# Kernel optimization log

Hardware: AMD Instinct MI355X
Metric: run time of the kernel (lower is better)

Reference implementation:

```python
import jax, jax.numpy as jnp
import numpy as np

EPS = 1e-6      # zero-token detection eps
LN_EPS = 1e-5   # torch LayerNorm default
H = 8           # num_heads


def setup_inputs() -> dict:
    key = jax.random.key(0)
    ks = jax.random.split(key, 6)
    B, T, D = 4, 2048, 512
    embs = jax.random.normal(ks[0], (B, T, D), jnp.float32)
    labels = jax.random.uniform(ks[1], (B, T), jnp.float32)
    s = 1.0 / np.sqrt(D)
    ln_g = jnp.ones((D,), jnp.float32)
    ln_b = jnp.zeros((D,), jnp.float32)
    in_proj_w = jax.random.uniform(ks[2], (3 * D, D), jnp.float32, -s, s)
    in_proj_b = jnp.zeros((3 * D,), jnp.float32)
    out_w = jax.random.uniform(ks[3], (D, D), jnp.float32, -s, s)
    out_b = jnp.zeros((D,), jnp.float32)
    alpha = jnp.float32(1.0)
    beta = jnp.float32(0.0)
    return {"embs": embs, "labels": labels, "ln_g": ln_g, "ln_b": ln_b,
            "in_proj_w": in_proj_w, "in_proj_b": in_proj_b,
            "out_w": out_w, "out_b": out_b, "alpha": alpha, "beta": beta}


def reference(embs, labels, ln_g, ln_b, in_proj_w, in_proj_b, out_w, out_b, alpha, beta):
    B, T, D = embs.shape
    h, dh = H, D // H
    # pre-LayerNorm
    mu = embs.mean(-1, keepdims=True)
    var = ((embs - mu) ** 2).mean(-1, keepdims=True)
    x = (embs - mu) / jnp.sqrt(var + LN_EPS) * ln_g + ln_b
    # key padding mask from all-zero tokens (computed on normalized x, as in source)
    kpm = jnp.abs(x).sum(-1) <= EPS                      # [B,T] bool
    w = jnp.where(kpm, jnp.float32(0.0), labels)         # zero labels on masked tokens
    # fused qkv projection (nn.MultiheadAttention in_proj)
    qkv = x @ in_proj_w.T + in_proj_b                    # [B,T,3D]
    q, k, v = jnp.split(qkv, 3, axis=-1)
    def sp(a):
        return a.reshape(B, T, h, dh).transpose(0, 2, 1, 3)  # [B,h,T,dh]
    q, k, v = sp(q), sp(k), sp(v)
    scores = jnp.einsum('bhqd,bhkd->bhqk', q, k) / np.sqrt(dh)
    # additive label bias: alpha * labels (broadcast over heads & queries) + beta
    scores = scores + (alpha * w[:, None, None, :] + beta)
    # key padding mask -> -inf (use large negative for stability)
    scores = jnp.where(kpm[:, None, None, :], jnp.float32(-1e30), scores)
    a = jax.nn.softmax(scores, axis=-1)
    o = jnp.einsum('bhqk,bhkd->bhqd', a, v).transpose(0, 2, 1, 3).reshape(B, T, D)
    o = o @ out_w.T + out_b
    o = jnp.nan_to_num(o, nan=0.0, posinf=0.0, neginf=0.0)
    # masked mean pool over T
    m = (~kpm)[..., None].astype(o.dtype)                # [B,T,1]
    pooled = (o * m).sum(1) / jnp.maximum(m.sum(1), 1.0)  # [B,D]
    return pooled
```

## Files before the change

### kernel.cpp

```cpp
#include <hip/hip_runtime.h>
#include <math.h>

#define T 2048
#define D 512
#define NH 8
#define DH 64
#define NB 4
#define NTOK (NB * T)
#define LOG2E 1.44269504f
#define QSCALE (0.125f * LOG2E)

using bf16x8 = __attribute__((ext_vector_type(8))) short;
using f32x4  = __attribute__((ext_vector_type(4))) float;

static __device__ __forceinline__ unsigned short f2bf(float f) {
    union { float f; unsigned u; } v; v.f = f;
    unsigned r = v.u + 0x7fffu + ((v.u >> 16) & 1u);
    return (unsigned short)(r >> 16);
}
#if __has_builtin(__builtin_amdgcn_cvt_pk_bf16_f32)
static __device__ __forceinline__ unsigned pack_bf16_pair(float a, float b) {
    auto r = __builtin_amdgcn_cvt_pk_bf16_f32(a, b);
    union { decltype(r) v; unsigned u; } c; c.v = r;
    return c.u;
}
#else
static __device__ __forceinline__ unsigned pack_bf16_pair(float a, float b) {
    union { float f; unsigned u; } ua, ub; ua.f = a; ub.f = b;
    unsigned ra = ua.u + 0x7fffu + ((ua.u >> 16) & 1u);
    unsigned rb = ub.u + 0x7fffu + ((ub.u >> 16) & 1u);
    return __builtin_amdgcn_perm(rb, ra, 0x07060302);
}
#endif


__global__ __launch_bounds__(256) void prep_kernel(
    const float* __restrict__ embs, const float* __restrict__ labels,
    const float* __restrict__ g, const float* __restrict__ bb,
    const float* __restrict__ alpha_p, const float* __restrict__ beta_p,
    const float* __restrict__ ipw,
    unsigned short* __restrict__ xfrag, float* __restrict__ wexp,
    float* __restrict__ kpmf, unsigned short* __restrict__ wbfrag,
    float* __restrict__ S)
{
    __shared__ __align__(16) unsigned short Sh[16][520];
    int blk = blockIdx.x;
    int tid = threadIdx.x, wave = tid >> 6, lane = tid & 63;
    int quad = lane >> 4, lm = lane & 15;

    if (blk >= 608) {
        float4 z = {0.f, 0.f, 0.f, 0.f};
        ((float4*)S)[tid] = z;
        ((float4*)S)[tid + 256] = z;
        return;
    }

    if (blk < 512) {
        int t16 = blk;
        float4 g0 = *(const float4*)(g + lane * 8), g1 = *(const float4*)(g + lane * 8 + 4);
        float4 c0 = *(const float4*)(bb + lane * 8), c1 = *(const float4*)(bb + lane * 8 + 4);
        float gv[8] = {g0.x, g0.y, g0.z, g0.w, g1.x, g1.y, g1.z, g1.w};
        float cv[8] = {c0.x, c0.y, c0.z, c0.w, c1.x, c1.y, c1.z, c1.w};

        for (int tt = 0; tt < 4; ++tt) {
            int n = t16 * 16 + wave * 4 + tt;
            const float* e = embs + (size_t)n * D + lane * 8;
            float4 a4 = *(const float4*)e, b4 = *(const float4*)(e + 4);
            float v[8] = {a4.x, a4.y, a4.z, a4.w, b4.x, b4.y, b4.z, b4.w};

            float s = 0.f, ss = 0.f;
            #pragma unroll
            for (int j = 0; j < 8; ++j) { s += v[j]; ss += v[j] * v[j]; }
            #pragma unroll
            for (int o = 1; o <= 32; o <<= 1) {
                s += __shfl_xor(s, o, 64);
                ss += __shfl_xor(ss, o, 64);
            }
            float mu = s * (1.0f / D);
            float var = ss * (1.0f / D) - mu * mu;
            float rstd = rsqrtf(var + 1e-5f);

            float x[8], as = 0.f;
            #pragma unroll
            for (int j = 0; j < 8; ++j) {
                x[j] = (v[j] - mu) * rstd * gv[j] + cv[j];
                as += fabsf(x[j]);
            }
            uint4 pk;
            pk.x = pack_bf16_pair(x[0], x[1]);
            pk.y = pack_bf16_pair(x[2], x[3]);
            pk.z = pack_bf16_pair(x[4], x[5]);
            pk.w = pack_bf16_pair(x[6], x[7]);
            *(uint4*)&Sh[wave * 4 + tt][lane * 8] = pk;

            #pragma unroll
            for (int o = 1; o <= 32; o <<= 1) as += __shfl_xor(as, o, 64);
            if (lane == 0) {
                int kpm = (as <= 1e-6f);
                kpmf[n] = kpm ? 1.0f : 0.0f;
                wexp[n] = kpm ? 0.0f : __expf(alpha_p[0] * labels[n] + beta_p[0]);
            }
        }
        __syncthreads();
        #pragma unroll
        for (int i = 0; i < 4; ++i) {
            int kc = wave * 4 + i;
            bf16x8 fr = *(const bf16x8*)&Sh[lm][kc * 32 + quad * 8];
            *(bf16x8*)(xfrag + ((size_t)(t16 * 16 + kc) * 64 + lane) * 8) = fr;
        }
    } else {
        int j16 = blk - 512;
        for (int tt = 0; tt < 4; ++tt) {
            int j = j16 * 16 + wave * 4 + tt;
            const float* wp = ipw + (size_t)j * D + lane * 8;
            float4 a4 = *(const float4*)wp, b4 = *(const float4*)(wp + 4);
            uint4 pk;
            pk.x = pack_bf16_pair(a4.x, a4.y);
            pk.y = pack_bf16_pair(a4.z, a4.w);
            pk.z = pack_bf16_pair(b4.x, b4.y);
            pk.w = pack_bf16_pair(b4.z, b4.w);
            *(uint4*)&Sh[wave * 4 + tt][lane * 8] = pk;
        }
        __syncthreads();
        #pragma unroll
        for (int i = 0; i < 4; ++i) {
            int kc = wave * 4 + i;
            bf16x8 fr = *(const bf16x8*)&Sh[lm][kc * 32 + quad * 8];
            *(bf16x8*)(wbfrag + ((size_t)(j16 * 16 + kc) * 64 + lane) * 8) = fr;
        }
    }
}

union QkvLds {
    struct { unsigned short A[2][8][512]; unsigned short B[2][8][512]; } st;
    unsigned short Ls[4][64][72];
};
__global__ __launch_bounds__(256) void qkv_mfma(
    const unsigned short* __restrict__ xfrag, const unsigned short* __restrict__ wbfrag,
    const float* __restrict__ bias, const float* __restrict__ wexp,
    unsigned short* __restrict__ qfrag, unsigned short* __restrict__ kfrag,
    unsigned short* __restrict__ vfrag)
{
    __shared__ __align__(16) QkvLds u;
    int tid = threadIdx.x;
    int wave = tid >> 6, lane = tid & 63, quad = lane >> 4, lm = lane & 15;
    int wr = wave >> 1, wc = wave & 1;
    int bx8 = blockIdx.x * 8, by8 = blockIdx.y * 8;
    int m0 = blockIdx.x * 128 + wr * 64;
    int j0 = blockIdx.y * 128 + wc * 64;

    f32x4 acc[4][4];
    #pragma unroll
    for (int a = 0; a < 4; ++a)
        #pragma unroll
        for (int b = 0; b < 4; ++b) acc[a][b] = (f32x4){0.f,0.f,0.f,0.f};

    auto stage = [&](int kc, int buf) {
        #pragma unroll
        for (int c = 0; c < 2; ++c) {
            int ci = wave * 2 + c;
            const unsigned short* ga = xfrag + ((size_t)((bx8 + ci) * 16 + kc) * 64 + lane) * 8;
            const unsigned short* gb = wbfrag + ((size_t)((by8 + ci) * 16 + kc) * 64 + lane) * 8;
            __builtin_amdgcn_global_load_lds(
                (const __attribute__((address_space(1))) void*)ga,
                (__attribute__((address_space(3))) void*)&u.st.A[buf][ci][0], 16, 0, 0);
            __builtin_amdgcn_global_load_lds(
                (const __attribute__((address_space(1))) void*)gb,
                (__attribute__((address_space(3))) void*)&u.st.B[buf][ci][0], 16, 0, 0);
        }
    };

    stage(0, 0);
    int buf = 0;
    for (int kc = 0; kc < 16; ++kc) {
        __syncthreads();
        if (kc < 15) stage(kc + 1, buf ^ 1);
        bf16x8 af[4], bf[4];
        #pragma unroll
        for (int mf = 0; mf < 4; ++mf)
            af[mf] = *(const bf16x8*)&u.st.A[buf][wr * 4 + mf][lane * 8];
        #pragma unroll
        for (int nt = 0; nt < 4; ++nt)
            bf[nt] = *(const bf16x8*)&u.st.B[buf][wc * 4 + nt][lane * 8];
        #pragma unroll
        for (int mf = 0; mf < 4; ++mf)
            #pragma unroll
            for (int nt = 0; nt < 4; ++nt)
                acc[mf][nt] = __builtin_amdgcn_mfma_f32_16x16x32_bf16(af[mf], bf[nt], acc[mf][nt], 0, 0, 0);
        buf ^= 1;
    }
    __syncthreads();

    int part = j0 >> 9;
    int h = (j0 & 511) >> 6;
    int b_ = m0 >> 11, tloc = m0 & (T - 1);
    int bh = b_ * NH + h;
    float bcol[4];
    #pragma unroll
    for (int nt = 0; nt < 4; ++nt) bcol[nt] = bias[j0 + nt * 16 + lm];

    if (part == 2) {
        float wv[4][4];
        #pragma unroll
        for (int mf = 0; mf < 4; ++mf)
            #pragma unroll
            for (int r = 0; r < 4; ++r)
                wv[mf][r] = wexp[b_ * T + tloc + mf * 16 + quad * 4 + r];
        #pragma unroll
        for (int mf = 0; mf < 4; ++mf)
            #pragma unroll
            for (int nt = 0; nt < 4; ++nt) {
                uint2 pw;
                pw.x = pack_bf16_pair((acc[mf][nt][0] + bcol[nt]) * wv[mf][0],
                                      (acc[mf][nt][1] + bcol[nt]) * wv[mf][1]);
                pw.y = pack_bf16_pair((acc[mf][nt][2] + bcol[nt]) * wv[mf][2],
                                      (acc[mf][nt][3] + bcol[nt]) * wv[mf][3]);
                *(uint2*)&u.Ls[wave][nt * 16 + lm][mf * 16 + quad * 4] = pw;
            }
        __syncthreads();
        #pragma unroll
        for (int nt = 0; nt < 4; ++nt)
            #pragma unroll
            for (int kk = 0; kk < 2; ++kk) {
                bf16x8 fr = *(const bf16x8*)&u.Ls[wave][nt * 16 + lm][kk * 32 + quad * 8];
                size_t chunk = ((((size_t)bh * 32 + (tloc >> 6)) * 2 + kk) * 5) + nt;
                *(bf16x8*)(vfrag + chunk * 512 + lane * 8) = fr;
            }
        #pragma unroll
        for (int kk = 0; kk < 2; ++kk) {
            size_t chunk = ((((size_t)bh * 32 + (tloc >> 6)) * 2 + kk) * 5) + 4;
            uint4 pk = {0u, 0u, 0u, 0u};
            if (lm == 0) {
                const float* wp = wexp + b_ * T + tloc + kk * 32 + quad * 8;
                unsigned short vv[8];
                #pragma unroll
                for (int e = 0; e < 8; ++e) vv[e] = f2bf(wp[e]);
                pk = *(uint4*)vv;
            }
            *(uint4*)(vfrag + chunk * 512 + (size_t)lane * 8) = pk;
        }
    } else {
        float scale = (part == 0) ? QSCALE : 1.0f;
        #pragma unroll
        for (int mf = 0; mf < 4; ++mf)
            #pragma unroll
            for (int nt = 0; nt < 4; ++nt)
                #pragma unroll
                for (int r = 0; r < 4; ++r)
                    u.Ls[wave][mf * 16 + quad * 4 + r][nt * 16 + lm] =
                        f2bf((acc[mf][nt][r] + bcol[nt]) * scale);
        __syncthreads();
        if (part == 0) {
            #pragma unroll
            for (int mf = 0; mf < 4; ++mf)
                #pragma unroll
                for (int kk = 0; kk < 2; ++kk) {
                    bf16x8 fr = *(const bf16x8*)&u.Ls[wave][mf * 16 + lm][kk * 32 + quad * 8];
                    size_t chunk = ((size_t)bh * 128 + (tloc >> 4) + mf) * 2 + kk;
                    *(bf16x8*)(qfrag + chunk * 512 + lane * 8) = fr;
                }
        } else {
            #pragma unroll
            for (int nta = 0; nta < 4; ++nta)
                #pragma unroll
                for (int kk = 0; kk < 2; ++kk) {
                    bf16x8 fr = *(const bf16x8*)&u.Ls[wave][lm * 4 + nta][kk * 32 + quad * 8];
                    size_t chunk = ((((size_t)bh * 32 + (tloc >> 6)) * 2 + kk) * 4) + nta;
                    *(bf16x8*)(kfrag + chunk * 512 + lane * 8) = fr;
                }
        }
    }
}

__global__ __launch_bounds__(256, 2) void attn_mfma(
    const unsigned short* __restrict__ qfrag, const unsigned short* __restrict__ kfrag,
    const unsigned short* __restrict__ vfrag, const float* __restrict__ kpmf,
    float* __restrict__ S)
{
    __shared__ __align__(16) unsigned short Ps[4][2][64][72];
    __shared__ float Lx[2][2][64];
    int g = blockIdx.x;
    int bh = g & 31, q0 = (g >> 5) * 128;
    int tid = threadIdx.x, wave = tid >> 6, lane = tid & 63;
    int quad = lane >> 4, lm = lane & 15;
    int qh = wave >> 1, ks = wave & 1;
    int qbase = q0 + qh * 64;
    int b_ = bh >> 3, h = bh & 7;

    bf16x8 qf[4][2];
    int t16b = (qbase >> 4);
    #pragma unroll
    for (int mf = 0; mf < 4; ++mf)
        #pragma unroll
        for (int kk = 0; kk < 2; ++kk)
            qf[mf][kk] = *(const bf16x8*)(qfrag +
                (((size_t)(bh * 128 + t16b + mf) * 2 + kk) * 64 + lane) * 8);

    f32x4 accO[4][4], accL[4];
    #pragma unroll
    for (int mf = 0; mf < 4; ++mf) {
        #pragma unroll
        for (int nt = 0; nt < 4; ++nt) accO[mf][nt] = (f32x4){0.f,0.f,0.f,0.f};
        accL[mf] = (f32x4){0.f,0.f,0.f,0.f};
    }

    const unsigned short* kb = kfrag + (size_t)bh * 32 * 8 * 512 + (size_t)lane * 8;
    const unsigned short* vb = vfrag + (size_t)bh * 32 * 10 * 512 + (size_t)lane * 8;
    int t0k = ks * 16;

    bf16x8 kf[4][2];
    auto load_k = [&](int t64) {
        const unsigned short* p = kb + (size_t)t64 * 8 * 512;
        #pragma unroll
        for (int kk = 0; kk < 2; ++kk)
            #pragma unroll
            for (int nt = 0; nt < 4; ++nt)
                kf[nt][kk] = *(const bf16x8*)(p + ((size_t)kk * 4 + nt) * 512);
    };
    auto load_v = [&](int t64, bf16x8 (&vf)[5][2]) {
        const unsigned short* p = vb + (size_t)t64 * 10 * 512;
        #pragma unroll
        for (int kk = 0; kk < 2; ++kk)
            #pragma unroll
            for (int nt = 0; nt < 5; ++nt)
                vf[nt][kk] = *(const bf16x8*)(p + ((size_t)kk * 5 + nt) * 512);
    };
    auto load_p = [&](int buf, bf16x8 (&pf)[4][2]) {
        #pragma unroll
        for (int mf = 0; mf < 4; ++mf)
            #pragma unroll
            for (int kk = 0; kk < 2; ++kk)
                pf[mf][kk] = *(const bf16x8*)&Ps[wave][buf][mf * 16 + lm][kk * 32 + quad * 8];
    };
    auto qk_exp = [&](int buf) {
        #pragma unroll
        for (int mf = 0; mf < 4; ++mf) {
            f32x4 s[4];
            __builtin_amdgcn_s_setprio(1);
            #pragma unroll
            for (int nt = 0; nt < 4; ++nt) {
                f32x4 t0 = (f32x4){0.f,0.f,0.f,0.f};
                t0 = __builtin_amdgcn_mfma_f32_16x16x32_bf16(qf[mf][0], kf[nt][0], t0, 0, 0, 0);
                t0 = __builtin_amdgcn_mfma_f32_16x16x32_bf16(qf[mf][1], kf[nt][1], t0, 0, 0, 0);
                s[nt] = t0;
            }
            __builtin_amdgcn_s_setprio(0);
            int rowb = mf * 16 + quad * 4;
            #pragma unroll
            for (int r = 0; r < 4; ++r) {
                float p0 = __builtin_amdgcn_exp2f(s[0][r]);
                float p1 = __builtin_amdgcn_exp2f(s[1][r]);
                float p2 = __builtin_amdgcn_exp2f(s[2][r]);
                float p3 = __builtin_amdgcn_exp2f(s[3][r]);
                uint2 pw;
                pw.x = pack_bf16_pair(p0, p1);
                pw.y = pack_bf16_pair(p2, p3);
                *(uint2*)&Ps[wave][buf][rowb + r][lm * 4] = pw;
            }
        }
    };
    auto pv = [&](bf16x8 (&pf)[4][2], bf16x8 (&vf)[5][2]) {
        __builtin_amdgcn_s_setprio(1);
        #pragma unroll
        for (int mf = 0; mf < 4; ++mf) {
            #pragma unroll
            for (int nt = 0; nt < 4; ++nt) {
                accO[mf][nt] = __builtin_amdgcn_mfma_f32_16x16x32_bf16(pf[mf][0], vf[nt][0], accO[mf][nt], 0, 0, 0);
                accO[mf][nt] = __builtin_amdgcn_mfma_f32_16x16x32_bf16(pf[mf][1], vf[nt][1], accO[mf][nt], 0, 0, 0);
            }
            accL[mf] = __builtin_amdgcn_mfma_f32_16x16x32_bf16(pf[mf][0], vf[4][0], accL[mf], 0, 0, 0);
            accL[mf] = __builtin_amdgcn_mfma_f32_16x16x32_bf16(pf[mf][1], vf[4][1], accL[mf], 0, 0, 0);
        }
        __builtin_amdgcn_s_setprio(0);
    };

    load_k(t0k);
    qk_exp(0);
    load_k(t0k + 1);
    for (int t = 1; t < 16; ++t) {
        bf16x8 pf[4][2], vf[5][2];
        load_p((t - 1) & 1, pf);
        load_v(t0k + t - 1, vf);
        qk_exp(t & 1);
        load_k(t0k + ((t + 1) & 15));
        pv(pf, vf);
    }
    {
        bf16x8 pf[4][2], vf[5][2];
        load_p(1, pf);
        load_v(t0k + 15, vf);
        pv(pf, vf);
    }

    if (lm == 0) {
        #pragma unroll
        for (int mf = 0; mf < 4; ++mf)
            #pragma unroll
            for (int r = 0; r < 4; ++r)
                Lx[qh][ks][mf * 16 + quad * 4 + r] = accL[mf][r];
    }
    __syncthreads();

    float pooled[4] = {0.f, 0.f, 0.f, 0.f};
    #pragma unroll
    for (int mf = 0; mf < 4; ++mf)
        #pragma unroll
        for (int r = 0; r < 4; ++r) {
            int rloc = mf * 16 + quad * 4 + r;
            float l = Lx[qh][0][rloc] + Lx[qh][1][rloc];
            float w = (1.0f - kpmf[b_ * T + qbase + rloc]) / l;
            #pragma unroll
            for (int nt = 0; nt < 4; ++nt) pooled[nt] += accO[mf][nt][r] * w;
        }
    #pragma unroll
    for (int nt = 0; nt < 4; ++nt) {
        pooled[nt] += __shfl_xor(pooled[nt], 16, 64);
        pooled[nt] += __shfl_xor(pooled[nt], 32, 64);
    }
    if (quad == 0) {
        #pragma unroll
        for (int nt = 0; nt < 4; ++nt)
            atomicAdd(&S[b_ * D + h * DH + nt * 16 + lm], pooled[nt]);
    }
}

__global__ __launch_bounds__(256) void out_kernel(
    const float* __restrict__ S, const float* __restrict__ kpmf,
    const float* __restrict__ Wo, const float* __restrict__ bo,
    float* __restrict__ out)
{
    __shared__ float Sl[512];
    __shared__ float cs[4];
    __shared__ float pr[4][64];
    int b_ = blockIdx.x >> 3;
    int cg = blockIdx.x & 7;
    int tid = threadIdx.x;
    int col = tid & 63, kq = tid >> 6;
    Sl[tid] = S[b_ * D + tid];
    Sl[tid + 256] = S[b_ * D + tid + 256];
    const float* kp = kpmf + b_ * T;
    float c = 0.f;
    for (int t = tid; t < T; t += 256) c += kp[t];
    #pragma unroll
    for (int o = 32; o; o >>= 1) c += __shfl_xor(c, o, 64);
    if ((tid & 63) == 0) cs[tid >> 6] = c;
    __syncthreads();
    float masked = cs[0] + cs[1] + cs[2] + cs[3];
    float cnt = (float)T - masked;
    float inv = 1.0f / fmaxf(cnt, 1.0f);

    int d = cg * 64 + col;
    const float4* wr4 = (const float4*)(Wo + (size_t)d * D + kq * 128);
    float dot = 0.f;
    #pragma unroll 8
    for (int i = 0; i < 32; ++i) {
        float4 w4 = wr4[i];
        int kbase = kq * 128 + i * 4;
        dot += Sl[kbase + 0] * w4.x + Sl[kbase + 1] * w4.y +
               Sl[kbase + 2] * w4.z + Sl[kbase + 3] * w4.w;
    }
    pr[kq][col] = dot;
    __syncthreads();
    if (kq == 0) {
        float tot = pr[0][col] + pr[1][col] + pr[2][col] + pr[3][col];
        out[b_ * D + d] = (tot + bo[d] * cnt) * inv;
    }
}

extern "C" void kernel_launch(void* const* d_in, const int* in_sizes, int n_in,
                              void* d_out, int out_size, void* d_ws, size_t ws_size,
                              hipStream_t stream) {
    const float* embs   = (const float*)d_in[0];
    const float* labels = (const float*)d_in[1];
    const float* ln_g   = (const float*)d_in[2];
    const float* ln_b   = (const float*)d_in[3];
    const float* ipw    = (const float*)d_in[4];
    const float* ipb    = (const float*)d_in[5];
    const float* ow     = (const float*)d_in[6];
    const float* obb    = (const float*)d_in[7];
    const float* alpha  = (const float*)d_in[8];
    const float* beta   = (const float*)d_in[9];
    float* out = (float*)d_out;

    unsigned short* xfrag  = (unsigned short*)d_ws;
    unsigned short* wbfrag = xfrag + (size_t)NTOK * D;
    unsigned short* qfrag  = wbfrag + (size_t)3 * D * D;
    unsigned short* kfrag  = qfrag + (size_t)NTOK * D;
    unsigned short* vfrag  = kfrag + (size_t)NTOK * D;
    float* wexp = (float*)(vfrag + (size_t)32 * 32 * 2 * 5 * 512);
    float* kpmf = wexp + NTOK;
    float* S    = kpmf + NTOK;

    prep_kernel<<<609, 256, 0, stream>>>(embs, labels, ln_g, ln_b, alpha, beta,
                                         ipw, xfrag, wexp, kpmf, wbfrag, S);
    dim3 gq(NTOK / 128, (3 * D) / 128);
    qkv_mfma<<<gq, 256, 0, stream>>>(xfrag, wbfrag, ipb, wexp, qfrag, kfrag, vfrag);
    attn_mfma<<<32 * (T / 128), 256, 0, stream>>>(qfrag, kfrag, vfrag, kpmf, S);
    out_kernel<<<NB * 8, 256, 0, stream>>>(S, kpmf, ow, obb, out);
}
```

Measured before the change: 151.0 us.

## Fuse output projection into attention kernel via global completion counter

Removes the separate out_kernel launch by having every attention block increment a global atomic counter after its pooled atomicAdds. The first 32 blocks then spin until all 512 blocks have finished and compute the output projection from S, reusing the attention shared memory through a union. This saves one kernel launch and its gap, but relies on all blocks making forward progress and adds spin-wait latency in the final blocks.

```diff
diff --git a/kernel.cpp b/kernel.cpp
--- a/kernel.cpp
+++ b/kernel.cpp
@@ -41,7 +41,7 @@
     const float* __restrict__ ipw,
     unsigned short* __restrict__ xfrag, float* __restrict__ wexp,
     float* __restrict__ kpmf, unsigned short* __restrict__ wbfrag,
-    float* __restrict__ S)
+    float* __restrict__ S, int* __restrict__ cnt)
 {
     __shared__ __align__(16) unsigned short Sh[16][520];
     int blk = blockIdx.x;
@@ -52,6 +52,7 @@
         float4 z = {0.f, 0.f, 0.f, 0.f};
         ((float4*)S)[tid] = z;
         ((float4*)S)[tid + 256] = z;
+        if (tid == 0) *cnt = 0;
         return;
     }
 
@@ -272,15 +273,20 @@
     }
 }
 
+union AttnU {
+    struct { unsigned short Ps[4][2][64][72]; float Lx[2][2][64]; } a;
+    struct { float Sl[512]; float cs[4]; float pr[4][64]; } o;
+};
 __global__ __launch_bounds__(256, 2) void attn_mfma(
     const unsigned short* __restrict__ qfrag, const unsigned short* __restrict__ kfrag,
     const unsigned short* __restrict__ vfrag, const float* __restrict__ kpmf,
-    float* __restrict__ S)
+    float* S, int* cnt,
+    const float* __restrict__ Wo, const float* __restrict__ bo,
+    float* __restrict__ out)
 {
-    __shared__ __align__(16) unsigned short Ps[4][2][64][72];
-    __shared__ float Lx[2][2][64];
-    int g = blockIdx.x;
-    int bh = g & 31, q0 = (g >> 5) * 128;
+    __shared__ __align__(16) AttnU u;
+    int gidx = blockIdx.x;
+    int bh = gidx & 31, q0 = (gidx >> 5) * 128;
     int tid = threadIdx.x, wave = tid >> 6, lane = tid & 63;
     int quad = lane >> 4, lm = lane & 15;
     int qh = wave >> 1, ks = wave & 1;
@@ -330,7 +336,7 @@
         for (int mf = 0; mf < 4; ++mf)
             #pragma unroll
             for (int kk = 0; kk < 2; ++kk)
-                pf[mf][kk] = *(const bf16x8*)&Ps[wave][buf][mf * 16 + lm][kk * 32 + quad * 8];
+                pf[mf][kk] = *(const bf16x8*)&u.a.Ps[wave][buf][mf * 16 + lm][kk * 32 + quad * 8];
     };
     auto qk_exp = [&](int buf) {
         #pragma unroll
@@ -355,7 +361,7 @@
                 uint2 pw;
                 pw.x = pack_bf16_pair(p0, p1);
                 pw.y = pack_bf16_pair(p2, p3);
-                *(uint2*)&Ps[wave][buf][rowb + r][lm * 4] = pw;
+                *(uint2*)&u.a.Ps[wave][buf][rowb + r][lm * 4] = pw;
             }
         }
     };
@@ -397,7 +403,7 @@
         for (int mf = 0; mf < 4; ++mf)
             #pragma unroll
             for (int r = 0; r < 4; ++r)
-                Lx[qh][ks][mf * 16 + quad * 4 + r] = accL[mf][r];
+                u.a.Lx[qh][ks][mf * 16 + quad * 4 + r] = accL[mf][r];
     }
     __syncthreads();
 
@@ -407,7 +413,7 @@
         #pragma unroll
         for (int r = 0; r < 4; ++r) {
             int rloc = mf * 16 + quad * 4 + r;
-            float l = Lx[qh][0][rloc] + Lx[qh][1][rloc];
+            float l = u.a.Lx[qh][0][rloc] + u.a.Lx[qh][1][rloc];
             float w = (1.0f - kpmf[b_ * T + qbase + rloc]) / l;
             #pragma unroll
             for (int nt = 0; nt < 4; ++nt) pooled[nt] += accO[mf][nt][r] * w;
@@ -422,48 +428,53 @@
         for (int nt = 0; nt < 4; ++nt)
             atomicAdd(&S[b_ * D + h * DH + nt * 16 + lm], pooled[nt]);
     }
-}
-
-__global__ __launch_bounds__(256) void out_kernel(
-    const float* __restrict__ S, const float* __restrict__ kpmf,
-    const float* __restrict__ Wo, const float* __restrict__ bo,
-    float* __restrict__ out)
-{
-    __shared__ float Sl[512];
-    __shared__ float cs[4];
-    __shared__ float pr[4][64];
-    int b_ = blockIdx.x >> 3;
-    int cg = blockIdx.x & 7;
-    int tid = threadIdx.x;
-    int col = tid & 63, kq = tid >> 6;
-    Sl[tid] = S[b_ * D + tid];
-    Sl[tid + 256] = S[b_ * D + tid + 256];
-    const float* kp = kpmf + b_ * T;
-    float c = 0.f;
-    for (int t = tid; t < T; t += 256) c += kp[t];
-    #pragma unroll
-    for (int o = 32; o; o >>= 1) c += __shfl_xor(c, o, 64);
-    if ((tid & 63) == 0) cs[tid >> 6] = c;
+
     __syncthreads();
-    float masked = cs[0] + cs[1] + cs[2] + cs[3];
-    float cnt = (float)T - masked;
-    float inv = 1.0f / fmaxf(cnt, 1.0f);
-
-    int d = cg * 64 + col;
-    const float4* wr4 = (const float4*)(Wo + (size_t)d * D + kq * 128);
-    float dot = 0.f;
-    #pragma unroll 8
-    for (int i = 0; i < 32; ++i) {
-        float4 w4 = wr4[i];
-        int kbase = kq * 128 + i * 4;
-        dot += Sl[kbase + 0] * w4.x + Sl[kbase + 1] * w4.y +
-               Sl[kbase + 2] * w4.z + Sl[kbase + 3] * w4.w;
-    }
-    pr[kq][col] = dot;
+    __threadfence();
+    if (tid == 0)
+        __hip_atomic_fetch_add(cnt, 1, __ATOMIC_ACQ_REL, __HIP_MEMORY_SCOPE_AGENT);
+    if (gidx >= 32) return;
+
+    if (tid == 0) {
+        while (__hip_atomic_load(cnt, __ATOMIC_ACQUIRE, __HIP_MEMORY_SCOPE_AGENT) < 512)
+            __builtin_amdgcn_s_sleep(8);
+    }
     __syncthreads();
-    if (kq == 0) {
-        float tot = pr[0][col] + pr[1][col] + pr[2][col] + pr[3][col];
-        out[b_ * D + d] = (tot + bo[d] * cnt) * inv;
+    {
+        int ob = gidx >> 3;
+        int cg = gidx & 7;
+        int col = tid & 63, kq = tid >> 6;
+        u.o.Sl[tid] = __hip_atomic_load(&S[ob * D + tid], __ATOMIC_RELAXED,
+                                        __HIP_MEMORY_SCOPE_AGENT);
+        u.o.Sl[tid + 256] = __hip_atomic_load(&S[ob * D + tid + 256], __ATOMIC_RELAXED,
+                                              __HIP_MEMORY_SCOPE_AGENT);
+        const float* kp = kpmf + ob * T;
+        float c = 0.f;
+        for (int t = tid; t < T; t += 256) c += kp[t];
+        #pragma unroll
+        for (int o = 32; o; o >>= 1) c += __shfl_xor(c, o, 64);
+        if ((tid & 63) == 0) u.o.cs[tid >> 6] = c;
+        __syncthreads();
+        float masked = u.o.cs[0] + u.o.cs[1] + u.o.cs[2] + u.o.cs[3];
+        float cnt_ = (float)T - masked;
+        float inv = 1.0f / fmaxf(cnt_, 1.0f);
+
+        int d = cg * 64 + col;
+        const float4* wr4 = (const float4*)(Wo + (size_t)d * D + kq * 128);
+        float dot = 0.f;
+        #pragma unroll 8
+        for (int i = 0; i < 32; ++i) {
+            float4 w4 = wr4[i];
+            int kbase = kq * 128 + i * 4;
+            dot += u.o.Sl[kbase + 0] * w4.x + u.o.Sl[kbase + 1] * w4.y +
+                   u.o.Sl[kbase + 2] * w4.z + u.o.Sl[kbase + 3] * w4.w;
+        }
+        u.o.pr[kq][col] = dot;
+        __syncthreads();
+        if (kq == 0) {
+            float tot = u.o.pr[0][col] + u.o.pr[1][col] + u.o.pr[2][col] + u.o.pr[3][col];
+            out[ob * D + d] = (tot + bo[d] * cnt_) * inv;
+        }
     }
 }
 
@@ -490,11 +501,12 @@
     float* wexp = (float*)(vfrag + (size_t)32 * 32 * 2 * 5 * 512);
     float* kpmf = wexp + NTOK;
     float* S    = kpmf + NTOK;
+    int*   cnt  = (int*)(S + NB * D);
 
     prep_kernel<<<609, 256, 0, stream>>>(embs, labels, ln_g, ln_b, alpha, beta,
-                                         ipw, xfrag, wexp, kpmf, wbfrag, S);
+                                         ipw, xfrag, wexp, kpmf, wbfrag, S, cnt);
     dim3 gq(NTOK / 128, (3 * D) / 128);
     qkv_mfma<<<gq, 256, 0, stream>>>(xfrag, wbfrag, ipb, wexp, qfrag, kfrag, vfrag);
-    attn_mfma<<<32 * (T / 128), 256, 0, stream>>>(qfrag, kfrag, vfrag, kpmf, S);
-    out_kernel<<<NB * 8, 256, 0, stream>>>(S, kpmf, ow, obb, out);
-}
+    attn_mfma<<<32 * (T / 128), 256, 0, stream>>>(qfrag, kfrag, vfrag, kpmf,
+                                                  S, cnt, ow, obb, out);
+}
```

Result: slower. 185.3 us (+22.7%).
